# Kernel optimization log

Hardware: AMD Instinct MI355X
Metric: run time of the kernel (lower is better)

## Reference

```python
import jax, jax.numpy as jnp
import numpy as np

B, H, W, T = 2, 48, 48, 48
DIM, NH, KS = 384, 6, 3
HD = DIM // NH
K3 = KS ** 3  # 27 local neighbors


def setup_inputs() -> dict:
    key = jax.random.key(0)
    k1, k2, k3 = jax.random.split(key, 3)
    q = jax.random.normal(k1, (B, H, W, T, DIM), dtype=jnp.float32)
    k = jax.random.normal(k2, (B, H, W, T, DIM), dtype=jnp.float32)
    rpb = jax.random.normal(k3, (NH, KS, KS, KS), dtype=jnp.float32) * 0.02
    # fixed displacement vectors: meshgrid of [-1, 0, 1]^3, 'ij' indexing -> (27, 3)
    vec = jnp.arange(-(KS // 2), KS // 2 + 1, dtype=jnp.float32)
    grid = jnp.stack(jnp.meshgrid(vec, vec, vec, indexing='ij'), axis=-1)
    v = grid.reshape(K3, 3)
    return {"q": q, "k": k, "rpb": rpb, "v": v}


def reference(q, k, rpb, v):
    scale = HD ** (-0.5)
    # (B,H,W,T,NH,HD), pre-scaled queries
    qh = q.reshape(B, H, W, T, NH, HD) * scale
    kh = k.reshape(B, H, W, T, NH, HD)
    pdr = KS // 2
    k_pad = jnp.pad(kh, ((0, 0), (pdr, pdr), (pdr, pdr), (pdr, pdr), (0, 0), (0, 0)))
    # local QK logits: for each of the 27 offsets, dot q with the shifted k.
    # Loop is over a fixed tiny neighborhood (27), not over data dims, and
    # avoids materializing a [27,B,H,W,T,C] gather tensor.
    logits = []
    for di in range(KS):
        for dj in range(KS):
            for dl in range(KS):
                ks = k_pad[:, di:di + H, dj:dj + W, dl:dl + T]  # (B,H,W,T,NH,HD)
                logits.append(jnp.einsum('bxyznd,bxyznd->bxyzn', qh, ks))
    attn = jnp.stack(logits, axis=-1)  # (B,H,W,T,NH,27)
    attn = attn + rpb.reshape(NH, K3)  # relative position bias
    attn = jax.nn.softmax(attn, axis=-1)
    # weighted sum of fixed displacement vectors: (B,H,W,T,NH,3)
    x = jnp.einsum('bxyzno,oc->bxyznc', attn, v)
    x = x.reshape(B, H, W, T, NH * 3)
    return x.transpose(0, 4, 1, 2, 3)  # (B, NH*3, H, W, T)
```

## Files before the change

kernel.cpp:

```cpp
#include <hip/hip_runtime.h>

namespace {

constexpr int DIM = 384;
constexpr int NH  = 6;
constexpr float L2E    = 1.44269504088896f;
constexpr float SCALE2 = 0.125f * L2E;

constexpr int TILES = 12 * 12 * 12;
constexpr int NBLK  = 2 * NH * TILES;

typedef _Float16 half8  __attribute__((ext_vector_type(8)));
typedef _Float16 half2v __attribute__((ext_vector_type(2)));
typedef __fp16   fp16x2 __attribute__((ext_vector_type(2)));
typedef float    floatx4 __attribute__((ext_vector_type(4)));
typedef unsigned uintx4 __attribute__((ext_vector_type(4)));

__device__ __forceinline__ half2v pk(float a, float b) {
    fp16x2 t = __builtin_amdgcn_cvt_pkrtz(a, b);
    return __builtin_bit_cast(half2v, t);
}

__device__ __forceinline__ uintx4 cvt_mask(const floatx4& u0, const floatx4& u1,
                                           unsigned m) {
    half8 h;
    ((half2v*)&h)[0] = pk(u0[0], u0[1]);
    ((half2v*)&h)[1] = pk(u0[2], u0[3]);
    ((half2v*)&h)[2] = pk(u1[0], u1[1]);
    ((half2v*)&h)[3] = pk(u1[2], u1[3]);
    uintx4 hv = __builtin_bit_cast(uintx4, h);
    const uintx4 m4 = {m, m, m, m};
    return hv & m4;
}

__global__ __launch_bounds__(256)
__attribute__((amdgpu_waves_per_eu(2, 4)))
void natten_reg(const float* __restrict__ q, const float* __restrict__ k,
                const float* __restrict__ rpb, float* __restrict__ out)
{
    __shared__ _Float16 k_lds[224 * 64];
    __shared__ unsigned tbl_lds[7 * 256];
    __shared__ float    rpbL[32];

    const int bid0 = blockIdx.x;
    const int bid  = (bid0 & 7) * (NBLK / 8) + (bid0 >> 3);
    const int n    = bid % NH;
    const int tile = (bid / NH) % TILES;
    const int b    = bid / (NH * TILES);
    const int tz = (tile % 12) * 4;
    const int ty = ((tile / 12) % 12) * 4;
    const int tx = (tile / 144) * 4;

    const int tid = threadIdx.x;
    const int w = tid >> 6, lane = tid & 63;
    const int lrow = lane & 15, lgrp = lane >> 4;
    char* kl = (char*)k_lds;

    if (tid < 32) rpbL[tid] = (tid < 27) ? rpb[n * 27 + tid] * L2E : -1e30f;

    #pragma unroll
    for (int i = 0; i < 7; ++i) {
        const int u  = 16 * i + ((tid >> 6) << 2) + (tid & 3);
        const int lr = (tid >> 2) & 15;
        unsigned val = 124u | 0x01010100u;
        if (u < 108) {
            const int rx = u / 36, rem = u - rx * 36;
            const int ry = rem / 6, rz = rem - ry * 6;
            const int dj = ry - (lr >> 2), dl = rz - (lr & 3);
            if ((unsigned)dj <= 2u && (unsigned)dl <= 2u)
                val = (unsigned)(((rx * 9 + dj * 3 + dl) << 2)
                      | (rx << 8) | (dj << 16) | (dl << 24));
        }
        tbl_lds[i * 256 + tid] = val;
    }

    const float* kb = k + (size_t)b * 110592 * DIM + n * 64;
    const int col0 = tid >> 3, ch = tid & 7;
    char* dst = kl + col0 * 128 + ((ch * 16) ^ ((col0 & 7) << 4));
    const float* ks[7];
    unsigned     um[7];
    {
        int cx = 0, cy = col0 / 6, cz = col0 - (col0 / 6) * 6;
        #pragma unroll
        for (int it = 0; it < 7; ++it) {
            const int gx = tx + cx - 1, gy = ty + cy - 1, gz = tz + cz - 1;
            const bool v = ((unsigned)gx < 48u) && ((unsigned)gy < 48u) &&
                           ((unsigned)gz < 48u);
            const int cgx = min(max(gx, 0), 47);
            const int cgy = min(max(gy, 0), 47);
            const int cgz = min(max(gz, 0), 47);
            ks[it] = kb + ((cgx * 48 + cgy) * 48 + cgz) * DIM + ch * 8;
            um[it] = v ? 0xFFFFFFFFu : 0u;
            cz += 2; if (cz >= 6) { cz -= 6; cy += 1; }
            cy += 5; if (cy >= 6) { cy -= 6; cx += 1; }
        }
    }
    const int qyo = lrow >> 2, qzo = lrow & 3;
    const float* qp = q + ((size_t)b * 110592
        + (size_t)(((tx + w) * 48 + (ty + qyo)) * 48 + (tz + qzo))) * DIM
        + n * 64 + lgrp * 8;

    __syncthreads();

    floatx4 F0[7], F1[7], Q0, Q1, Q2, Q3;
    #pragma unroll
    for (int it = 0; it < 7; ++it) {
        asm volatile(
            "global_load_dwordx4 %0, %2, off\n\t"
            "global_load_dwordx4 %1, %2, off offset:16"
            : "=&v"(F0[it]), "=&v"(F1[it]) : "v"(ks[it]) : "memory");
    }
    asm volatile(
        "global_load_dwordx4 %0, %4, off\n\t"
        "global_load_dwordx4 %1, %4, off offset:16\n\t"
        "global_load_dwordx4 %2, %4, off offset:128\n\t"
        "global_load_dwordx4 %3, %4, off offset:144"
        : "=&v"(Q0), "=&v"(Q1), "=&v"(Q2), "=&v"(Q3) : "v"(qp) : "memory");

    asm volatile("s_waitcnt vmcnt(8)"
        : "+v"(F0[0]), "+v"(F0[1]), "+v"(F0[2]), "+v"(F0[3]), "+v"(F0[4]),
          "+v"(F1[0]), "+v"(F1[1]), "+v"(F1[2]), "+v"(F1[3]), "+v"(F1[4]) ::);
    __builtin_amdgcn_sched_barrier(0);
    #pragma unroll
    for (int it = 0; it < 5; ++it)
        *(uintx4*)(dst + it * 4096) = cvt_mask(F0[it], F1[it], um[it]);

    asm volatile("s_waitcnt vmcnt(0)"
        : "+v"(F0[5]), "+v"(F0[6]), "+v"(F1[5]), "+v"(F1[6]),
          "+v"(Q0), "+v"(Q1), "+v"(Q2), "+v"(Q3) ::);
    __builtin_amdgcn_sched_barrier(0);
    #pragma unroll
    for (int it = 5; it < 7; ++it)
        *(uintx4*)(dst + it * 4096) = cvt_mask(F0[it], F1[it], um[it]);

    half8 a0, a1;
    ((half2v*)&a0)[0] = pk(Q0[0], Q0[1]); ((half2v*)&a0)[1] = pk(Q0[2], Q0[3]);
    ((half2v*)&a0)[2] = pk(Q1[0], Q1[1]); ((half2v*)&a0)[3] = pk(Q1[2], Q1[3]);
    ((half2v*)&a1)[0] = pk(Q2[0], Q2[1]); ((half2v*)&a1)[1] = pk(Q2[2], Q2[3]);
    ((half2v*)&a1)[2] = pk(Q3[0], Q3[1]); ((half2v*)&a1)[3] = pk(Q3[2], Q3[3]);
    __syncthreads();

    uintx4 tr[7];
    #pragma unroll
    for (int j = 0; j < 7; ++j)
        tr[j] = *(const uintx4*)&tbl_lds[j * 256 + lgrp * 64 + lrow * 4];

    const int cbase = w * 36 + lrow;
    const int xm2 = (cbase & 7) << 4;
    const char* bpA = kl + cbase * 128 + ((lgrp * 16) ^ xm2);
    const char* bpB = kl + cbase * 128 + ((lgrp * 16 + 64) ^ xm2);
    floatx4 acc[7];
    #pragma unroll
    for (int j = 0; j < 7; ++j) {
        const half8 b0 = *(const half8*)(bpA + j * 2048);
        const half8 b1 = *(const half8*)(bpB + j * 2048);
        floatx4 c = {0.f, 0.f, 0.f, 0.f};
        c = __builtin_amdgcn_mfma_f32_16x16x32_f16(b0, a0, c, 0, 0, 0);
        c = __builtin_amdgcn_mfma_f32_16x16x32_f16(b1, a1, c, 0, 0, 0);
        acc[j] = c;
    }

    float den = 0.f, sx = 0.f, sy = 0.f, sz = 0.f;
    #pragma unroll
    for (int j = 0; j < 7; ++j) {
        #pragma unroll
        for (int r = 0; r < 4; ++r) {
            const unsigned t = tr[j][r];
            const float bias = *(const float*)((const char*)rpbL + (t & 124u));
            const float e = __builtin_amdgcn_exp2f(fmaf(acc[j][r], SCALE2, bias));
            den += e;
            sx = fmaf(e, (float)((t >> 8) & 255u), sx);
            sy = fmaf(e, (float)((t >> 16) & 255u), sy);
            sz = fmaf(e, (float)(t >> 24), sz);
        }
    }
    den += __shfl_xor(den, 16); den += __shfl_xor(den, 32);
    sx  += __shfl_xor(sx, 16);  sx  += __shfl_xor(sx, 32);
    sy  += __shfl_xor(sy, 16);  sy  += __shfl_xor(sy, 32);
    sz  += __shfl_xor(sz, 16);  sz  += __shfl_xor(sz, 32);

    if (lgrp < 3) {
        const float s = (lgrp == 0) ? sx : (lgrp == 1 ? sy : sz);
        const float res = s / den - 1.0f;
        out[((size_t)(b * 18 + n * 3 + lgrp) * 48 + (tx + w)) * 2304
            + (size_t)(ty + qyo) * 48 + (tz + qzo)] = res;
    }
}

}

extern "C" void kernel_launch(void* const* d_in, const int* in_sizes, int n_in,
                              void* d_out, int out_size, void* d_ws, size_t ws_size,
                              hipStream_t stream)
{
    (void)in_sizes; (void)n_in; (void)d_ws; (void)ws_size; (void)out_size;
    const float* q   = (const float*)d_in[0];
    const float* k   = (const float*)d_in[1];
    const float* rpb = (const float*)d_in[2];
    float* out = (float*)d_out;

    natten_reg<<<dim3(NBLK), dim3(256), 0, stream>>>(q, k, rpb, out);
}
```

Before: 211.1 us.

## Enlarge spatial tile to 4x4x8 with 512-thread blocks to cut K halo reloads

Doubles each block's query tile along z (4x4x8) and uses 512 threads, so the K halo is 6x6x10 columns per block instead of 6x6x6 per 4x4x4 tile. This lowers redundant K fetches from global memory per output point. The neighbor-column lookup for the MFMA B operand is now computed from constant offset tables instead of a fixed stride. The explicit inline-asm load pipelining with staged waitcnt is replaced by plain loads, which may expose more memory latency. The larger blocks also change occupancy.

Result: faster. 182.4 us (-13.6%).

```diff
diff --git a/kernel.cpp b/kernel.cpp
--- a/kernel.cpp
+++ b/kernel.cpp
@@ -7,8 +7,9 @@
 constexpr float L2E    = 1.44269504088896f;
 constexpr float SCALE2 = 0.125f * L2E;
 
-constexpr int TILES = 12 * 12 * 12;
+constexpr int TILES = 12 * 12 * 6;
 constexpr int NBLK  = 2 * NH * TILES;
+constexpr int NCOL  = 6 * 6 * 10;
 
 typedef _Float16 half8  __attribute__((ext_vector_type(8)));
 typedef _Float16 half2v __attribute__((ext_vector_type(2)));
@@ -21,24 +22,15 @@
     return __builtin_bit_cast(half2v, t);
 }
 
-__device__ __forceinline__ uintx4 cvt_mask(const floatx4& u0, const floatx4& u1,
-                                           unsigned m) {
-    half8 h;
-    ((half2v*)&h)[0] = pk(u0[0], u0[1]);
-    ((half2v*)&h)[1] = pk(u0[2], u0[3]);
-    ((half2v*)&h)[2] = pk(u1[0], u1[1]);
-    ((half2v*)&h)[3] = pk(u1[2], u1[3]);
-    uintx4 hv = __builtin_bit_cast(uintx4, h);
-    const uintx4 m4 = {m, m, m, m};
-    return hv & m4;
-}
+__device__ constexpr int Nx[7] = {0, 0, 0, 1, 1, 2, 2};
+__device__ constexpr int Ny[7] = {0, 2, 5, 2, 4, 1, 4};
+__device__ constexpr int Nz[7] = {0, 4, 2, 0, 4, 2, 0};
 
-__global__ __launch_bounds__(256)
-__attribute__((amdgpu_waves_per_eu(2, 4)))
-void natten_reg(const float* __restrict__ q, const float* __restrict__ k,
-                const float* __restrict__ rpb, float* __restrict__ out)
+__global__ __launch_bounds__(512, 2)
+void natten_z8(const float* __restrict__ q, const float* __restrict__ k,
+               const float* __restrict__ rpb, float* __restrict__ out)
 {
-    __shared__ _Float16 k_lds[224 * 64];
+    __shared__ _Float16 k_lds[NCOL * 64];
     __shared__ unsigned tbl_lds[7 * 256];
     __shared__ float    rpbL[32];
 
@@ -47,9 +39,9 @@
     const int n    = bid % NH;
     const int tile = (bid / NH) % TILES;
     const int b    = bid / (NH * TILES);
-    const int tz = (tile % 12) * 4;
-    const int ty = ((tile / 12) % 12) * 4;
-    const int tx = (tile / 144) * 4;
+    const int tz = (tile % 6) * 8;
+    const int ty = ((tile / 6) % 12) * 4;
+    const int tx = (tile / 72) * 4;
 
     const int tid = threadIdx.x;
     const int w = tid >> 6, lane = tid & 63;
@@ -59,113 +51,106 @@
     if (tid < 32) rpbL[tid] = (tid < 27) ? rpb[n * 27 + tid] * L2E : -1e30f;
 
     #pragma unroll
-    for (int i = 0; i < 7; ++i) {
-        const int u  = 16 * i + ((tid >> 6) << 2) + (tid & 3);
-        const int lr = (tid >> 2) & 15;
-        unsigned val = 124u | 0x01010100u;
-        if (u < 108) {
-            const int rx = u / 36, rem = u - rx * 36;
-            const int ry = rem / 6, rz = rem - ry * 6;
-            const int dj = ry - (lr >> 2), dl = rz - (lr & 3);
-            if ((unsigned)dj <= 2u && (unsigned)dl <= 2u)
-                val = (unsigned)(((rx * 9 + dj * 3 + dl) << 2)
-                      | (rx << 8) | (dj << 16) | (dl << 24));
+    for (int i = 0; i < 4; ++i) {
+        const int e = i * 512 + tid;
+        if (e < 1792) {
+            const int j = e >> 8;
+            const int u = j * 16 + (((e >> 6) & 3) << 2) + (e & 3);
+            const int lr = (e >> 2) & 15;
+            unsigned val = 124u | 0x01010100u;
+            if (u < 108) {
+                const int rx = u / 36, rem = u - rx * 36;
+                const int ry = rem / 6, rz = rem - ry * 6;
+                const int dj = ry - (lr >> 2), dl = rz - (lr & 3);
+                if ((unsigned)dj <= 2u && (unsigned)dl <= 2u)
+                    val = (unsigned)(((rx * 9 + dj * 3 + dl) << 2)
+                          | (rx << 8) | (dj << 16) | (dl << 24));
+            }
+            tbl_lds[e] = val;
         }
-        tbl_lds[i * 256 + tid] = val;
     }
 
     const float* kb = k + (size_t)b * 110592 * DIM + n * 64;
-    const int col0 = tid >> 3, ch = tid & 7;
-    char* dst = kl + col0 * 128 + ((ch * 16) ^ ((col0 & 7) << 4));
-    const float* ks[7];
-    unsigned     um[7];
     {
-        int cx = 0, cy = col0 / 6, cz = col0 - (col0 / 6) * 6;
+        const int col0 = tid >> 3, ch = tid & 7;
+        int cx = col0 / 60, rem = col0 - cx * 60;
+        int cy = rem / 10, cz = rem - cy * 10;
+        char* dst = kl + col0 * 128 + ((ch * 16) ^ ((col0 & 7) << 4));
         #pragma unroll
-        for (int it = 0; it < 7; ++it) {
-            const int gx = tx + cx - 1, gy = ty + cy - 1, gz = tz + cz - 1;
-            const bool v = ((unsigned)gx < 48u) && ((unsigned)gy < 48u) &&
-                           ((unsigned)gz < 48u);
-            const int cgx = min(max(gx, 0), 47);
-            const int cgy = min(max(gy, 0), 47);
-            const int cgz = min(max(gz, 0), 47);
-            ks[it] = kb + ((cgx * 48 + cgy) * 48 + cgz) * DIM + ch * 8;
-            um[it] = v ? 0xFFFFFFFFu : 0u;
-            cz += 2; if (cz >= 6) { cz -= 6; cy += 1; }
-            cy += 5; if (cy >= 6) { cy -= 6; cx += 1; }
+        for (int it = 0; it < 6; ++it) {
+            if (col0 + it * 64 < NCOL) {
+                const int gx = tx + cx - 1, gy = ty + cy - 1, gz = tz + cz - 1;
+                const bool v = ((unsigned)gx < 48u) && ((unsigned)gy < 48u) &&
+                               ((unsigned)gz < 48u);
+                const int cgx = min(max(gx, 0), 47);
+                const int cgy = min(max(gy, 0), 47);
+                const int cgz = min(max(gz, 0), 47);
+                const float* s = kb + ((cgx * 48 + cgy) * 48 + cgz) * DIM + ch * 8;
+                const float4 f0 = ((const float4*)s)[0];
+                const float4 f1 = ((const float4*)s)[1];
+                const unsigned m = v ? 0xFFFFFFFFu : 0u;
+                half8 h;
+                ((half2v*)&h)[0] = pk(f0.x, f0.y);
+                ((half2v*)&h)[1] = pk(f0.z, f0.w);
+                ((half2v*)&h)[2] = pk(f1.x, f1.y);
+                ((half2v*)&h)[3] = pk(f1.z, f1.w);
+                uintx4 hv = __builtin_bit_cast(uintx4, h);
+                const uintx4 m4 = {m, m, m, m};
+                hv &= m4;
+                *(uintx4*)(dst + it * 8192) = hv;
+            }
+            cz += 4; if (cz >= 10) { cz -= 10; cy += 1; }
+            cx += 1; if (cy >= 6)  { cy -= 6;  cx += 1; }
         }
     }
-    const int qyo = lrow >> 2, qzo = lrow & 3;
-    const float* qp = q + ((size_t)b * 110592
-        + (size_t)(((tx + w) * 48 + (ty + qyo)) * 48 + (tz + qzo))) * DIM
-        + n * 64 + lgrp * 8;
 
+    const int mx = w >> 1, mz = (w & 1) * 4;
+    const int qy = lrow >> 2, qz = lrow & 3;
+    half8 a0, a1;
+    {
+        const float* qp = q + ((size_t)b * 110592
+            + (size_t)(((tx + mx) * 48 + (ty + qy)) * 48 + (tz + mz + qz))) * DIM
+            + n * 64 + lgrp * 8;
+        const float4 f0 = ((const float4*)qp)[0];
+        const float4 f1 = ((const float4*)qp)[1];
+        const float4 g0 = ((const float4*)(qp + 32))[0];
+        const float4 g1 = ((const float4*)(qp + 32))[1];
+        ((half2v*)&a0)[0] = pk(f0.x, f0.y); ((half2v*)&a0)[1] = pk(f0.z, f0.w);
+        ((half2v*)&a0)[2] = pk(f1.x, f1.y); ((half2v*)&a0)[3] = pk(f1.z, f1.w);
+        ((half2v*)&a1)[0] = pk(g0.x, g0.y); ((half2v*)&a1)[1] = pk(g0.z, g0.w);
+        ((half2v*)&a1)[2] = pk(g1.x, g1.y); ((half2v*)&a1)[3] = pk(g1.z, g1.w);
+    }
     __syncthreads();
 
-    floatx4 F0[7], F1[7], Q0, Q1, Q2, Q3;
-    #pragma unroll
-    for (int it = 0; it < 7; ++it) {
-        asm volatile(
-            "global_load_dwordx4 %0, %2, off\n\t"
-            "global_load_dwordx4 %1, %2, off offset:16"
-            : "=&v"(F0[it]), "=&v"(F1[it]) : "v"(ks[it]) : "memory");
-    }
-    asm volatile(
-        "global_load_dwordx4 %0, %4, off\n\t"
-        "global_load_dwordx4 %1, %4, off offset:16\n\t"
-        "global_load_dwordx4 %2, %4, off offset:128\n\t"
-        "global_load_dwordx4 %3, %4, off offset:144"
-        : "=&v"(Q0), "=&v"(Q1), "=&v"(Q2), "=&v"(Q3) : "v"(qp) : "memory");
-
-    asm volatile("s_waitcnt vmcnt(8)"
-        : "+v"(F0[0]), "+v"(F0[1]), "+v"(F0[2]), "+v"(F0[3]), "+v"(F0[4]),
-          "+v"(F1[0]), "+v"(F1[1]), "+v"(F1[2]), "+v"(F1[3]), "+v"(F1[4]) ::);
-    __builtin_amdgcn_sched_barrier(0);
-    #pragma unroll
-    for (int it = 0; it < 5; ++it)
-        *(uintx4*)(dst + it * 4096) = cvt_mask(F0[it], F1[it], um[it]);
-
-    asm volatile("s_waitcnt vmcnt(0)"
-        : "+v"(F0[5]), "+v"(F0[6]), "+v"(F1[5]), "+v"(F1[6]),
-          "+v"(Q0), "+v"(Q1), "+v"(Q2), "+v"(Q3) ::);
-    __builtin_amdgcn_sched_barrier(0);
-    #pragma unroll
-    for (int it = 5; it < 7; ++it)
-        *(uintx4*)(dst + it * 4096) = cvt_mask(F0[it], F1[it], um[it]);
-
-    half8 a0, a1;
-    ((half2v*)&a0)[0] = pk(Q0[0], Q0[1]); ((half2v*)&a0)[1] = pk(Q0[2], Q0[3]);
-    ((half2v*)&a0)[2] = pk(Q1[0], Q1[1]); ((half2v*)&a0)[3] = pk(Q1[2], Q1[3]);
-    ((half2v*)&a1)[0] = pk(Q2[0], Q2[1]); ((half2v*)&a1)[1] = pk(Q2[2], Q2[3]);
-    ((half2v*)&a1)[2] = pk(Q3[0], Q3[1]); ((half2v*)&a1)[3] = pk(Q3[2], Q3[3]);
-    __syncthreads();
-
-    uintx4 tr[7];
-    #pragma unroll
-    for (int j = 0; j < 7; ++j)
-        tr[j] = *(const uintx4*)&tbl_lds[j * 256 + lgrp * 64 + lrow * 4];
-
-    const int cbase = w * 36 + lrow;
-    const int xm2 = (cbase & 7) << 4;
-    const char* bpA = kl + cbase * 128 + ((lgrp * 16) ^ xm2);
-    const char* bpB = kl + cbase * 128 + ((lgrp * 16 + 64) ^ xm2);
+    const int ly6 = lrow >= 12 ? 2 : (lrow >= 6 ? 1 : 0);
+    const int lz6 = lrow - ly6 * 6;
+    const int cw = mx * 60 + mz;
     floatx4 acc[7];
     #pragma unroll
     for (int j = 0; j < 7; ++j) {
-        const half8 b0 = *(const half8*)(bpA + j * 2048);
-        const half8 b1 = *(const half8*)(bpB + j * 2048);
-        floatx4 c = {0.f, 0.f, 0.f, 0.f};
-        c = __builtin_amdgcn_mfma_f32_16x16x32_f16(b0, a0, c, 0, 0, 0);
-        c = __builtin_amdgcn_mfma_f32_16x16x32_f16(b1, a1, c, 0, 0, 0);
-        acc[j] = c;
+        int rz = lz6 + Nz[j];
+        int ry = ly6 + Ny[j];
+        if (rz >= 6) { rz -= 6; ry += 1; }
+        int rx = Nx[j];
+        if (ry >= 6) { ry -= 6; rx += 1; }
+        const int c = min(cw + rx * 60 + ry * 10 + rz, NCOL - 1);
+        const char* base = kl + c * 128;
+        const unsigned xm = (unsigned)(c & 7) << 4;
+        const half8 b0 = *(const half8*)(base + ((lgrp * 16) ^ xm));
+        const half8 b1 = *(const half8*)(base + ((lgrp * 16 + 64) ^ xm));
+        floatx4 cc = {0.f, 0.f, 0.f, 0.f};
+        cc = __builtin_amdgcn_mfma_f32_16x16x32_f16(b0, a0, cc, 0, 0, 0);
+        cc = __builtin_amdgcn_mfma_f32_16x16x32_f16(b1, a1, cc, 0, 0, 0);
+        acc[j] = cc;
     }
 
     float den = 0.f, sx = 0.f, sy = 0.f, sz = 0.f;
     #pragma unroll
     for (int j = 0; j < 7; ++j) {
+        const uintx4 tr = *(const uintx4*)&tbl_lds[j * 256 + lgrp * 64 + lrow * 4];
         #pragma unroll
         for (int r = 0; r < 4; ++r) {
-            const unsigned t = tr[j][r];
+            const unsigned t = tr[r];
             const float bias = *(const float*)((const char*)rpbL + (t & 124u));
             const float e = __builtin_amdgcn_exp2f(fmaf(acc[j][r], SCALE2, bias));
             den += e;
@@ -182,8 +167,8 @@
     if (lgrp < 3) {
         const float s = (lgrp == 0) ? sx : (lgrp == 1 ? sy : sz);
         const float res = s / den - 1.0f;
-        out[((size_t)(b * 18 + n * 3 + lgrp) * 48 + (tx + w)) * 2304
-            + (size_t)(ty + qyo) * 48 + (tz + qzo)] = res;
+        out[((size_t)(b * 18 + n * 3 + lgrp) * 48 + (tx + mx)) * 2304
+            + (size_t)(ty + qy) * 48 + (tz + mz + qz)] = res;
     }
 }
 
@@ -199,5 +184,5 @@
     const float* rpb = (const float*)d_in[2];
     float* out = (float*)d_out;
 
-    natten_reg<<<dim3(NBLK), dim3(256), 0, stream>>>(q, k, rpb, out);
+    natten_z8<<<dim3(NBLK), dim3(512), 0, stream>>>(q, k, rpb, out);
 }
```
